# Kernel optimization log

Hardware: AMD Instinct MI355X
Metric: run time of the kernel (lower is better)

Reference implementation:

```python
import jax, jax.numpy as jnp
import numpy as np

COMMITMENT_COST = 0.25
NUM_EMBEDDINGS = 512
EMBEDDING_DIM = 128


def setup_inputs() -> dict:
    key = jax.random.key(0)
    k1, k2 = jax.random.split(key)
    z = jax.random.normal(k1, (64, 128, 32, 32), dtype=jnp.float32)
    # nn.Embedding weight initialized uniform(-1/K, 1/K)
    lim = 1.0 / NUM_EMBEDDINGS
    emb_weight = jax.random.uniform(
        k2, (NUM_EMBEDDINGS, EMBEDDING_DIM), dtype=jnp.float32,
        minval=-lim, maxval=lim)
    return {"z": z, "emb_weight": emb_weight}


def reference(z, emb_weight):
    b, c, h, w = z.shape  # c == embedding_dim
    # (b, h, w, c) -> (b*h*w, c)
    z_cl = jnp.transpose(z, (0, 2, 3, 1))
    z_flat = z_cl.reshape(b * h * w, c)
    # squared L2 distances: ||z||^2 + ||e||^2 - 2 z.e  -> [N, K]
    distances = (
        jnp.sum(z_flat ** 2, axis=-1, keepdims=True)
        + jnp.sum(emb_weight ** 2, axis=-1)[None, :]
        - 2.0 * jnp.matmul(z_flat, emb_weight.T)
    )
    encoding_indices = jnp.argmin(distances, axis=-1)  # [N]
    z_q = emb_weight[encoding_indices]                 # [N, c]
    z_q = z_q.reshape(b, h, w, c)
    z_q = jnp.transpose(z_q, (0, 3, 1, 2))             # [b, c, h, w]
    loss = (
        jnp.mean((z_q - jax.lax.stop_gradient(z)) ** 2)
        + COMMITMENT_COST * jnp.mean((jax.lax.stop_gradient(z_q) - z) ** 2)
    )
    # straight-through estimator
    z_q_st = z + jax.lax.stop_gradient(z_q - z)
    return (z_q_st, loss, encoding_indices)
```

## Files before the change

kernel.cpp:

```cpp
#include <hip/hip_runtime.h>


#define D_DIM 128
#define HW    1024
#define GAP_THR 2.5e-4f
#define FLAG_CAP 16384

typedef short short8 __attribute__((ext_vector_type(8)));
typedef float f32x16 __attribute__((ext_vector_type(16)));

union U8 { unsigned int u[4]; short8 s; uint4 q; };

__device__ __forceinline__ unsigned short f2bf(float v) {
    unsigned int u = __builtin_bit_cast(unsigned int, v);
    return (unsigned short)((u + 0x7fffu + ((u >> 16) & 1u)) >> 16);
}
__device__ __forceinline__ float bfhi(unsigned short h) {
    unsigned int u = ((unsigned int)h) << 16;
    return __builtin_bit_cast(float, u);
}
__device__ __forceinline__ unsigned int umn(unsigned int a, unsigned int b) {
    return a < b ? a : b;
}
__device__ __forceinline__ unsigned int umx(unsigned int a, unsigned int b) {
    return a > b ? a : b;
}

__global__ void prep_kernel(const float* __restrict__ emb,
                            float* __restrict__ etr,
                            uint4* __restrict__ ebh, uint4* __restrict__ ebl,
                            float* __restrict__ se) {
    const int t = blockIdx.x * 256 + threadIdx.x;

    {
        const int k = t >> 7;
        const int d = t & 127;
        etr[d * 512 + k] = emb[t];
    }

    if (t < 8192) {
        const int lane = t & 63;
        const int ks   = (t >> 6) & 7;
        const int kcol = t >> 9;
        const int krow = kcol * 32 + (lane & 31);
        const int d0   = ks * 16 + (lane >> 5) * 8;
        const float* ep = emb + (size_t)krow * D_DIM + d0;
        float v[8];
        #pragma unroll
        for (int j = 0; j < 8; ++j) v[j] = ep[j];
        U8 hh, ll;
        #pragma unroll
        for (int p = 0; p < 4; ++p) {
            const unsigned short h0 = f2bf(v[2*p]), h1 = f2bf(v[2*p+1]);
            const unsigned short l0 = f2bf(v[2*p]   - bfhi(h0));
            const unsigned short l1 = f2bf(v[2*p+1] - bfhi(h1));
            hh.u[p] = (unsigned int)h0 | ((unsigned int)h1 << 16);
            ll.u[p] = (unsigned int)l0 | ((unsigned int)l1 << 16);
        }
        ebh[t] = hh.q;
        ebl[t] = ll.q;
    }

    if (t < 512) {
        const float* e = emb + (size_t)t * D_DIM;
        float r[8];
        #pragma unroll
        for (int j = 0; j < 8; ++j) {
            float v = e[j];
            float p = v * v;
            asm("" : "+v"(p));
            r[j] = p;
        }
        for (int i = 8; i < 128; i += 8) {
            #pragma unroll
            for (int j = 0; j < 8; ++j) {
                float v = e[i + j];
                float p = v * v;
                asm("" : "+v"(p));
                r[j] += p;
            }
        }
        se[t] = ((r[0] + r[1]) + (r[2] + r[3])) + ((r[4] + r[5]) + (r[6] + r[7]));
    }
}

__launch_bounds__(256, 1)
__global__ void dist_kernel(const float* __restrict__ z,
                            const uint4* __restrict__ ebh,
                            const uint4* __restrict__ ebl,
                            const float* __restrict__ se_g,
                            const float* __restrict__ emb,
                            float* __restrict__ idx_out,
                            unsigned int* __restrict__ flag_cnt,
                            int* __restrict__ flag_list,
                            float* __restrict__ zq,
                            double* __restrict__ loss) {
    __shared__ unsigned int red1[4][32], red2[4][32];
    __shared__ int li_sh[32];
    __shared__ float ept[D_DIM * 33];
    __shared__ float lred[4];

    const int tid  = threadIdx.x;
    const int lane = tid & 63;
    const int wid  = tid >> 6;
    const int tile = blockIdx.x;
    const int row  = lane & 31;
    const int n0   = tile * 32;
    const int bimg = n0 >> 10;
    const int hw0  = n0 & 1023;

    short8 Ah[8], Al[8];
    {
        const float* zc = z + (size_t)bimg * (D_DIM * HW) + hw0 + row;
        #pragma unroll
        for (int ks = 0; ks < 8; ++ks) {
            const int d0 = ks * 16 + (lane >> 5) * 8;
            float v[8];
            #pragma unroll
            for (int j = 0; j < 8; ++j) v[j] = zc[(size_t)(d0 + j) * HW];
            U8 hh, ll;
            #pragma unroll
            for (int p = 0; p < 4; ++p) {
                unsigned int hwd, lwd;
                asm("v_cvt_pk_bf16_f32 %0, %1, %2" : "=v"(hwd) : "v"(v[2*p]), "v"(v[2*p+1]));
                const float xh = __builtin_bit_cast(float, hwd << 16);
                const float yh = __builtin_bit_cast(float, hwd & 0xffff0000u);
                const float xl = v[2*p]   - xh;
                const float yl = v[2*p+1] - yh;
                asm("v_cvt_pk_bf16_f32 %0, %1, %2" : "=v"(lwd) : "v"(xl), "v"(yl));
                hh.u[p] = hwd; ll.u[p] = lwd;
            }
            Ah[ks] = hh.s; Al[ks] = ll.s;
        }
    }

    unsigned int b1[16], b2[16];
    #pragma unroll
    for (int j = 0; j < 16; ++j) { b1[j] = 0xFFFFFFFFu; b2[j] = 0xFFFFFFFFu; }

    for (int i = 0; i < 4; ++i) {
        const int   kc   = wid * 4 + i;
        const int   kgl  = kc * 32 + row;
        const float sevp = se_g[kgl] + 0.5f;
        const uint4* pbh = ebh + kc * 512 + lane;
        const uint4* pbl = ebl + kc * 512 + lane;

        f32x16 a0, a1;
        #pragma unroll
        for (int j = 0; j < 16; ++j) { a0[j] = 0.f; a1[j] = 0.f; }

        #pragma unroll
        for (int ks = 0; ks < 8; ++ks) {
            U8 bh; bh.q = pbh[ks * 64];
            U8 bl; bl.q = pbl[ks * 64];
            if (ks & 1) {
                a1 = __builtin_amdgcn_mfma_f32_32x32x16_bf16(Ah[ks], bh.s, a1, 0, 0, 0);
                a1 = __builtin_amdgcn_mfma_f32_32x32x16_bf16(Ah[ks], bl.s, a1, 0, 0, 0);
                a1 = __builtin_amdgcn_mfma_f32_32x32x16_bf16(Al[ks], bh.s, a1, 0, 0, 0);
            } else {
                a0 = __builtin_amdgcn_mfma_f32_32x32x16_bf16(Ah[ks], bh.s, a0, 0, 0, 0);
                a0 = __builtin_amdgcn_mfma_f32_32x32x16_bf16(Ah[ks], bl.s, a0, 0, 0, 0);
                a0 = __builtin_amdgcn_mfma_f32_32x32x16_bf16(Al[ks], bh.s, a0, 0, 0, 0);
            }
        }

        #pragma unroll
        for (int j = 0; j < 16; ++j) {
            const float dot = a0[j] + a1[j];
            const float pd  = fmaf(-2.f, dot, sevp);
            const unsigned int key =
                (__builtin_bit_cast(unsigned int, pd) & 0xFFFFFE00u) | (unsigned int)kgl;
            const unsigned int m = umn(key, b1[j]);
            b2[j] = umn(umx(key, b1[j]), b2[j]);
            b1[j] = m;
        }
    }

    #pragma unroll
    for (int off = 1; off <= 16; off <<= 1) {
        #pragma unroll
        for (int j = 0; j < 16; ++j) {
            const unsigned int o1 = (unsigned int)__shfl_xor((int)b1[j], off);
            const unsigned int o2 = (unsigned int)__shfl_xor((int)b2[j], off);
            const unsigned int m  = umn(b1[j], o1);
            b2[j] = umn(umx(b1[j], o1), umn(b2[j], o2));
            b1[j] = m;
        }
    }

    if ((lane & 31) == 0) {
        const int half = lane >> 5;
        #pragma unroll
        for (int j = 0; j < 16; ++j) {
            const int r = (j & 3) + 8 * (j >> 2) + 4 * half;
            red1[wid][r] = b1[j];
            red2[wid][r] = b2[j];
        }
    }
    __syncthreads();

    if (tid < 32) {
        unsigned int m1 = red1[0][tid], m2 = red2[0][tid];
        #pragma unroll
        for (int w = 1; w < 4; ++w) {
            const unsigned int v1 = red1[w][tid];
            const unsigned int v2 = red2[w][tid];
            const unsigned int nm = umn(m1, v1);
            m2 = umn(umn(m2, v2), umx(m1, v1));
            m1 = nm;
        }
        const int n = n0 + tid;
        const int code = (int)(m1 & 511u);
        idx_out[n] = (float)code;
        li_sh[tid] = code;
        const float f1 = __builtin_bit_cast(float, m1 & 0xFFFFFE00u);
        const float f2 = __builtin_bit_cast(float, m2 & 0xFFFFFE00u);
        if (f2 - f1 < GAP_THR) {
            unsigned int p = atomicAdd(flag_cnt, 1u);
            if (p < FLAG_CAP) flag_list[p] = n;
        }
    }
    __syncthreads();

    {
        const int p   = tid >> 3;
        const int sub = tid & 7;
        const float* er = emb + (size_t)li_sh[p] * D_DIM + sub * 16;
        #pragma unroll
        for (int j4 = 0; j4 < 4; ++j4) {
            const float4 v = *(const float4*)(er + j4 * 4);
            const int c = sub * 16 + j4 * 4;
            ept[(c + 0) * 33 + p] = v.x;
            ept[(c + 1) * 33 + p] = v.y;
            ept[(c + 2) * 33 + p] = v.z;
            ept[(c + 3) * 33 + p] = v.w;
        }
    }
    __syncthreads();
    {
        const int p  = tid & 31;
        const int c0 = tid >> 5;
        const float* zb2 = z  + (size_t)bimg * (D_DIM * HW) + hw0 + p;
        float*       qb  = zq + (size_t)bimg * (D_DIM * HW) + hw0 + p;
        float lacc = 0.f;
        #pragma unroll
        for (int i = 0; i < 16; ++i) {
            const int c = c0 + i * 8;
            const float v  = ept[c * 33 + p];
            const float zv = zb2[(size_t)c * HW];
            qb[(size_t)c * HW] = v;
            const float df = v - zv;
            lacc = fmaf(df, df, lacc);
        }
        #pragma unroll
        for (int off = 32; off > 0; off >>= 1) lacc += __shfl_down(lacc, off);
        if (lane == 0) lred[wid] = lacc;
    }
    __syncthreads();
    if (tid == 0)
        atomicAdd(loss, (double)(lred[0] + lred[1] + lred[2] + lred[3]));
}

__launch_bounds__(512)
__global__ void fixup_kernel(const float* __restrict__ z,
                             const float* __restrict__ etr,
                             const unsigned int* __restrict__ flag_cnt,
                             const int* __restrict__ flag_list,
                             const float* __restrict__ se_np,
                             float* __restrict__ idx_out) {
    __shared__ float zrow[D_DIM];
    __shared__ float q[D_DIM];
    __shared__ float rsum[8];
    __shared__ float szs;
    __shared__ float rv[8];
    __shared__ int   rix[8];

    const int tid = threadIdx.x;
    unsigned int cnt = *flag_cnt;
    if (cnt > FLAG_CAP) cnt = FLAG_CAP;

    for (unsigned int f = blockIdx.x; f < cnt; f += gridDim.x) {
        const int row = flag_list[f];
        const int b   = row >> 10;
        const int hw  = row & 1023;
        __syncthreads();
        if (tid < D_DIM) {
            float v = z[(size_t)b * (D_DIM * HW) + (size_t)tid * HW + hw];
            zrow[tid] = v;
            q[tid] = v * v;
        }
        __syncthreads();
        if (tid < 8) {
            float r = q[tid];
            for (int i = 8; i < 128; i += 8) r += q[i + tid];
            rsum[tid] = r;
        }
        __syncthreads();
        if (tid == 0)
            szs = ((rsum[0] + rsum[1]) + (rsum[2] + rsum[3]))
                + ((rsum[4] + rsum[5]) + (rsum[6] + rsum[7]));
        __syncthreads();
        const float sz32 = szs;

        const int k = tid;
        double dot0 = 0.0, dot1 = 0.0;
        #pragma unroll 4
        for (int d = 0; d < D_DIM; d += 2) {
            dot0 += (double)etr[d * 512 + k]       * (double)zrow[d];
            dot1 += (double)etr[(d + 1) * 512 + k] * (double)zrow[d + 1];
        }
        const float dotf = (float)(dot0 + dot1);
        const float T    = sz32 + se_np[k];
        float best  = T - 2.0f * dotf;
        int   besti = k;

        #pragma unroll
        for (int off = 32; off > 0; off >>= 1) {
            const float ov = __shfl_down(best, off);
            const int   oi = __shfl_down(besti, off);
            if (ov < best || (ov == best && oi < besti)) { best = ov; besti = oi; }
        }
        if ((tid & 63) == 0) { rv[tid >> 6] = best; rix[tid >> 6] = besti; }
        __syncthreads();
        if (tid == 0) {
            #pragma unroll
            for (int w = 1; w < 8; ++w)
                if (rv[w] < best || (rv[w] == best && rix[w] < besti)) {
                    best = rv[w]; besti = rix[w];
                }
            idx_out[row] = (float)besti;
        }
    }
}

__global__ void fin_kernel(const double* __restrict__ loss, float* __restrict__ out_loss) {
    *out_loss = (float)(*loss * 1.25 / 8388608.0);
}

extern "C" void kernel_launch(void* const* d_in, const int* in_sizes, int n_in,
                              void* d_out, int out_size, void* d_ws, size_t ws_size,
                              hipStream_t stream) {
    const float* z   = (const float*)d_in[0];
    const float* emb = (const float*)d_in[1];
    float* out      = (float*)d_out;
    float* zq       = out;
    float* out_loss = out + 8388608;
    float* idx_f    = out + 8388609;

    char* ws = (char*)d_ws;
    unsigned int* flag_cnt = (unsigned int*)ws;
    double*       loss     = (double*)(ws + 8);
    float*        se       = (float*)(ws + 10240);
    uint4*        ebh      = (uint4*)(ws + 16384);
    uint4*        ebl      = (uint4*)(ws + 16384 + 131072);
    int*          flag_list= (int*)(ws + 16384 + 262144);
    float*        etr      = (float*)(ws + 16384 + 262144 + 65536);

    hipMemsetAsync(d_ws, 0, 16384, stream);
    prep_kernel <<<256,  256, 0, stream>>>(emb, etr, ebh, ebl, se);
    dist_kernel <<<2048, 256, 0, stream>>>(z, ebh, ebl, se, emb, idx_f,
                                           flag_cnt, flag_list, zq, loss);
    fixup_kernel<<<2048, 512, 0, stream>>>(z, etr, flag_cnt, flag_list, se, idx_f);
    fin_kernel  <<<1,    1,   0, stream>>>(loss, out_loss);
}
```

Measured before the change: 117.4 us.

## Give each wave its own 32 rows over all codes, dropping cross-wave argmin reduction

```diff
diff --git a/kernel.cpp b/kernel.cpp
--- a/kernel.cpp
+++ b/kernel.cpp
@@ -95,23 +95,23 @@
                             int* __restrict__ flag_list,
                             float* __restrict__ zq,
                             double* __restrict__ loss) {
-    __shared__ unsigned int red1[4][32], red2[4][32];
-    __shared__ int li_sh[32];
+    __shared__ int   li_sh[128];
     __shared__ float ept[D_DIM * 33];
     __shared__ float lred[4];
 
     const int tid  = threadIdx.x;
     const int lane = tid & 63;
     const int wid  = tid >> 6;
-    const int tile = blockIdx.x;
     const int row  = lane & 31;
-    const int n0   = tile * 32;
-    const int bimg = n0 >> 10;
-    const int hw0  = n0 & 1023;
+    const int nblk = blockIdx.x * 128;
+    const int bimg = nblk >> 10;
+    const int hw0  = nblk & 1023;
+    const int n0   = nblk + wid * 32;
+    const int hww  = hw0 + wid * 32;
 
     short8 Ah[8], Al[8];
     {
-        const float* zc = z + (size_t)bimg * (D_DIM * HW) + hw0 + row;
+        const float* zc = z + (size_t)bimg * (D_DIM * HW) + hww + row;
         #pragma unroll
         for (int ks = 0; ks < 8; ++ks) {
             const int d0 = ks * 16 + (lane >> 5) * 8;
@@ -138,35 +138,28 @@
     #pragma unroll
     for (int j = 0; j < 16; ++j) { b1[j] = 0xFFFFFFFFu; b2[j] = 0xFFFFFFFFu; }
 
-    for (int i = 0; i < 4; ++i) {
-        const int   kc   = wid * 4 + i;
+    for (int kc = 0; kc < 16; ++kc) {
         const int   kgl  = kc * 32 + row;
         const float sevp = se_g[kgl] + 0.5f;
         const uint4* pbh = ebh + kc * 512 + lane;
         const uint4* pbl = ebl + kc * 512 + lane;
 
-        f32x16 a0, a1;
-        #pragma unroll
-        for (int j = 0; j < 16; ++j) { a0[j] = 0.f; a1[j] = 0.f; }
+        f32x16 ahh, ahl, alh;
+        #pragma unroll
+        for (int j = 0; j < 16; ++j) { ahh[j] = 0.f; ahl[j] = 0.f; alh[j] = 0.f; }
 
         #pragma unroll
         for (int ks = 0; ks < 8; ++ks) {
             U8 bh; bh.q = pbh[ks * 64];
             U8 bl; bl.q = pbl[ks * 64];
-            if (ks & 1) {
-                a1 = __builtin_amdgcn_mfma_f32_32x32x16_bf16(Ah[ks], bh.s, a1, 0, 0, 0);
-                a1 = __builtin_amdgcn_mfma_f32_32x32x16_bf16(Ah[ks], bl.s, a1, 0, 0, 0);
-                a1 = __builtin_amdgcn_mfma_f32_32x32x16_bf16(Al[ks], bh.s, a1, 0, 0, 0);
-            } else {
-                a0 = __builtin_amdgcn_mfma_f32_32x32x16_bf16(Ah[ks], bh.s, a0, 0, 0, 0);
-                a0 = __builtin_amdgcn_mfma_f32_32x32x16_bf16(Ah[ks], bl.s, a0, 0, 0, 0);
-                a0 = __builtin_amdgcn_mfma_f32_32x32x16_bf16(Al[ks], bh.s, a0, 0, 0, 0);
-            }
+            ahh = __builtin_amdgcn_mfma_f32_32x32x16_bf16(Ah[ks], bh.s, ahh, 0, 0, 0);
+            ahl = __builtin_amdgcn_mfma_f32_32x32x16_bf16(Ah[ks], bl.s, ahl, 0, 0, 0);
+            alh = __builtin_amdgcn_mfma_f32_32x32x16_bf16(Al[ks], bh.s, alh, 0, 0, 0);
         }
 
         #pragma unroll
         for (int j = 0; j < 16; ++j) {
-            const float dot = a0[j] + a1[j];
+            const float dot = (ahh[j] + ahl[j]) + alh[j];
             const float pd  = fmaf(-2.f, dot, sevp);
             const unsigned int key =
                 (__builtin_bit_cast(unsigned int, pd) & 0xFFFFFE00u) | (unsigned int)kgl;
@@ -193,69 +186,57 @@
         #pragma unroll
         for (int j = 0; j < 16; ++j) {
             const int r = (j & 3) + 8 * (j >> 2) + 4 * half;
-            red1[wid][r] = b1[j];
-            red2[wid][r] = b2[j];
-        }
-    }
-    __syncthreads();
-
-    if (tid < 32) {
-        unsigned int m1 = red1[0][tid], m2 = red2[0][tid];
-        #pragma unroll
-        for (int w = 1; w < 4; ++w) {
-            const unsigned int v1 = red1[w][tid];
-            const unsigned int v2 = red2[w][tid];
-            const unsigned int nm = umn(m1, v1);
-            m2 = umn(umn(m2, v2), umx(m1, v1));
-            m1 = nm;
-        }
-        const int n = n0 + tid;
-        const int code = (int)(m1 & 511u);
-        idx_out[n] = (float)code;
-        li_sh[tid] = code;
-        const float f1 = __builtin_bit_cast(float, m1 & 0xFFFFFE00u);
-        const float f2 = __builtin_bit_cast(float, m2 & 0xFFFFFE00u);
-        if (f2 - f1 < GAP_THR) {
-            unsigned int p = atomicAdd(flag_cnt, 1u);
-            if (p < FLAG_CAP) flag_list[p] = n;
-        }
-    }
-    __syncthreads();
-
-    {
-        const int p   = tid >> 3;
-        const int sub = tid & 7;
-        const float* er = emb + (size_t)li_sh[p] * D_DIM + sub * 16;
-        #pragma unroll
-        for (int j4 = 0; j4 < 4; ++j4) {
-            const float4 v = *(const float4*)(er + j4 * 4);
-            const int c = sub * 16 + j4 * 4;
-            ept[(c + 0) * 33 + p] = v.x;
-            ept[(c + 1) * 33 + p] = v.y;
-            ept[(c + 2) * 33 + p] = v.z;
-            ept[(c + 3) * 33 + p] = v.w;
-        }
-    }
-    __syncthreads();
-    {
-        const int p  = tid & 31;
-        const int c0 = tid >> 5;
-        const float* zb2 = z  + (size_t)bimg * (D_DIM * HW) + hw0 + p;
-        float*       qb  = zq + (size_t)bimg * (D_DIM * HW) + hw0 + p;
-        float lacc = 0.f;
-        #pragma unroll
-        for (int i = 0; i < 16; ++i) {
-            const int c = c0 + i * 8;
-            const float v  = ept[c * 33 + p];
-            const float zv = zb2[(size_t)c * HW];
-            qb[(size_t)c * HW] = v;
-            const float df = v - zv;
-            lacc = fmaf(df, df, lacc);
-        }
-        #pragma unroll
-        for (int off = 32; off > 0; off >>= 1) lacc += __shfl_down(lacc, off);
-        if (lane == 0) lred[wid] = lacc;
-    }
+            const int n = n0 + r;
+            const int code = (int)(b1[j] & 511u);
+            idx_out[n] = (float)code;
+            li_sh[wid * 32 + r] = code;
+            const float f1 = __builtin_bit_cast(float, b1[j] & 0xFFFFFE00u);
+            const float f2 = __builtin_bit_cast(float, b2[j] & 0xFFFFFE00u);
+            if (f2 - f1 < GAP_THR) {
+                unsigned int p = atomicAdd(flag_cnt, 1u);
+                if (p < FLAG_CAP) flag_list[p] = n;
+            }
+        }
+    }
+
+    float lacc = 0.f;
+    for (int h = 0; h < 4; ++h) {
+        __syncthreads();
+        {
+            const int p   = tid >> 3;
+            const int sub = tid & 7;
+            const float* er = emb + (size_t)li_sh[h * 32 + p] * D_DIM + sub * 16;
+            #pragma unroll
+            for (int j4 = 0; j4 < 4; ++j4) {
+                const float4 v = *(const float4*)(er + j4 * 4);
+                const int c = sub * 16 + j4 * 4;
+                ept[(c + 0) * 33 + p] = v.x;
+                ept[(c + 1) * 33 + p] = v.y;
+                ept[(c + 2) * 33 + p] = v.z;
+                ept[(c + 3) * 33 + p] = v.w;
+            }
+        }
+        __syncthreads();
+        {
+            const int p  = tid & 31;
+            const int c0 = tid >> 5;
+            const int hwp = hw0 + h * 32 + p;
+            const float* zb2 = z  + (size_t)bimg * (D_DIM * HW) + hwp;
+            float*       qb  = zq + (size_t)bimg * (D_DIM * HW) + hwp;
+            #pragma unroll
+            for (int i = 0; i < 16; ++i) {
+                const int c = c0 + i * 8;
+                const float v  = ept[c * 33 + p];
+                const float zv = zb2[(size_t)c * HW];
+                qb[(size_t)c * HW] = v;
+                const float df = v - zv;
+                lacc = fmaf(df, df, lacc);
+            }
+        }
+    }
+    #pragma unroll
+    for (int off = 32; off > 0; off >>= 1) lacc += __shfl_down(lacc, off);
+    if (lane == 0) lred[wid] = lacc;
     __syncthreads();
     if (tid == 0)
         atomicAdd(loss, (double)(lred[0] + lred[1] + lred[2] + lred[3]));
@@ -358,7 +339,7 @@
 
     hipMemsetAsync(d_ws, 0, 16384, stream);
     prep_kernel <<<256,  256, 0, stream>>>(emb, etr, ebh, ebl, se);
-    dist_kernel <<<2048, 256, 0, stream>>>(z, ebh, ebl, se, emb, idx_f,
+    dist_kernel <<<512,  256, 0, stream>>>(z, ebh, ebl, se, emb, idx_f,
                                            flag_cnt, flag_list, zq, loss);
     fixup_kernel<<<2048, 512, 0, stream>>>(z, etr, flag_cnt, flag_list, se, idx_f);
     fin_kernel  <<<1,    1,   0, stream>>>(loss, out_loss);
```

After: 111.0 us. -5.4%, faster.

## Halve dist_kernel block to two waves, each scanning eight codebook chunks

Applied to the files above, without the earlier changes.

```diff
diff --git a/kernel.cpp b/kernel.cpp
--- a/kernel.cpp
+++ b/kernel.cpp
@@ -84,7 +84,7 @@
     }
 }
 
-__launch_bounds__(256, 1)
+__launch_bounds__(128, 1)
 __global__ void dist_kernel(const float* __restrict__ z,
                             const uint4* __restrict__ ebh,
                             const uint4* __restrict__ ebl,
@@ -95,19 +95,18 @@
                             int* __restrict__ flag_list,
                             float* __restrict__ zq,
                             double* __restrict__ loss) {
-    __shared__ unsigned int red1[4][32], red2[4][32];
-    __shared__ int li_sh[32];
+    __shared__ unsigned int red1[2][32], red2[2][32];
+    __shared__ int   li_sh[32];
     __shared__ float ept[D_DIM * 33];
-    __shared__ float lred[4];
+    __shared__ float lred[2];
 
     const int tid  = threadIdx.x;
     const int lane = tid & 63;
-    const int wid  = tid >> 6;
-    const int tile = blockIdx.x;
+    const int wk   = tid >> 6;
     const int row  = lane & 31;
-    const int n0   = tile * 32;
-    const int bimg = n0 >> 10;
-    const int hw0  = n0 & 1023;
+    const int nblk = blockIdx.x * 32;
+    const int bimg = nblk >> 10;
+    const int hw0  = nblk & 1023;
 
     short8 Ah[8], Al[8];
     {
@@ -138,8 +137,8 @@
     #pragma unroll
     for (int j = 0; j < 16; ++j) { b1[j] = 0xFFFFFFFFu; b2[j] = 0xFFFFFFFFu; }
 
-    for (int i = 0; i < 4; ++i) {
-        const int   kc   = wid * 4 + i;
+    for (int i = 0; i < 8; ++i) {
+        const int   kc   = wk * 8 + i;
         const int   kgl  = kc * 32 + row;
         const float sevp = se_g[kgl] + 0.5f;
         const uint4* pbh = ebh + kc * 512 + lane;
@@ -166,8 +165,7 @@
 
         #pragma unroll
         for (int j = 0; j < 16; ++j) {
-            const float dot = a0[j] + a1[j];
-            const float pd  = fmaf(-2.f, dot, sevp);
+            const float pd = fmaf(-2.f, a0[j], fmaf(-2.f, a1[j], sevp));
             const unsigned int key =
                 (__builtin_bit_cast(unsigned int, pd) & 0xFFFFFE00u) | (unsigned int)kgl;
             const unsigned int m = umn(key, b1[j]);
@@ -193,23 +191,18 @@
         #pragma unroll
         for (int j = 0; j < 16; ++j) {
             const int r = (j & 3) + 8 * (j >> 2) + 4 * half;
-            red1[wid][r] = b1[j];
-            red2[wid][r] = b2[j];
+            red1[wk][r] = b1[j];
+            red2[wk][r] = b2[j];
         }
     }
     __syncthreads();
 
     if (tid < 32) {
-        unsigned int m1 = red1[0][tid], m2 = red2[0][tid];
-        #pragma unroll
-        for (int w = 1; w < 4; ++w) {
-            const unsigned int v1 = red1[w][tid];
-            const unsigned int v2 = red2[w][tid];
-            const unsigned int nm = umn(m1, v1);
-            m2 = umn(umn(m2, v2), umx(m1, v1));
-            m1 = nm;
-        }
-        const int n = n0 + tid;
+        const unsigned int v1a = red1[0][tid], v2a = red2[0][tid];
+        const unsigned int v1b = red1[1][tid], v2b = red2[1][tid];
+        const unsigned int m1 = umn(v1a, v1b);
+        const unsigned int m2 = umn(umn(v2a, v2b), umx(v1a, v1b));
+        const int n = nblk + tid;
         const int code = (int)(m1 & 511u);
         idx_out[n] = (float)code;
         li_sh[tid] = code;
@@ -223,13 +216,13 @@
     __syncthreads();
 
     {
-        const int p   = tid >> 3;
-        const int sub = tid & 7;
-        const float* er = emb + (size_t)li_sh[p] * D_DIM + sub * 16;
-        #pragma unroll
-        for (int j4 = 0; j4 < 4; ++j4) {
+        const int p   = tid >> 2;
+        const int sub = tid & 3;
+        const float* er = emb + (size_t)li_sh[p] * D_DIM + sub * 32;
+        #pragma unroll
+        for (int j4 = 0; j4 < 8; ++j4) {
             const float4 v = *(const float4*)(er + j4 * 4);
-            const int c = sub * 16 + j4 * 4;
+            const int c = sub * 32 + j4 * 4;
             ept[(c + 0) * 33 + p] = v.x;
             ept[(c + 1) * 33 + p] = v.y;
             ept[(c + 2) * 33 + p] = v.z;
@@ -244,8 +237,8 @@
         float*       qb  = zq + (size_t)bimg * (D_DIM * HW) + hw0 + p;
         float lacc = 0.f;
         #pragma unroll
-        for (int i = 0; i < 16; ++i) {
-            const int c = c0 + i * 8;
+        for (int i = 0; i < 32; ++i) {
+            const int c = c0 + i * 4;
             const float v  = ept[c * 33 + p];
             const float zv = zb2[(size_t)c * HW];
             qb[(size_t)c * HW] = v;
@@ -254,11 +247,11 @@
         }
         #pragma unroll
         for (int off = 32; off > 0; off >>= 1) lacc += __shfl_down(lacc, off);
-        if (lane == 0) lred[wid] = lacc;
+        if (lane == 0) lred[wk] = lacc;
     }
     __syncthreads();
     if (tid == 0)
-        atomicAdd(loss, (double)(lred[0] + lred[1] + lred[2] + lred[3]));
+        atomicAdd(loss, (double)(lred[0] + lred[1]));
 }
 
 __launch_bounds__(512)
@@ -358,7 +351,7 @@
 
     hipMemsetAsync(d_ws, 0, 16384, stream);
     prep_kernel <<<256,  256, 0, stream>>>(emb, etr, ebh, ebl, se);
-    dist_kernel <<<2048, 256, 0, stream>>>(z, ebh, ebl, se, emb, idx_f,
+    dist_kernel <<<2048, 128, 0, stream>>>(z, ebh, ebl, se, emb, idx_f,
                                            flag_cnt, flag_list, zq, loss);
     fixup_kernel<<<2048, 512, 0, stream>>>(z, etr, flag_cnt, flag_list, se, idx_f);
     fin_kernel  <<<1,    1,   0, stream>>>(loss, out_loss);
```

New measurement: 124.3 us. 1.06x slower.
